# Optimization experiments

Measured on AMD Instinct MI355X. Metric: run time of the kernel, lower is better.

The kernel has to match this reference:

```python
import jax, jax.numpy as jnp
import numpy as np
import math

B, S, E, H = 4, 4096, 2048, 16
Dh = E // H  # 128


def setup_inputs() -> dict:
    key = jax.random.key(0)
    ks = jax.random.split(key, 8)
    s = 1.0 / math.sqrt(E)
    return {
        "x": jax.random.normal(ks[0], (B, S, E), dtype=jnp.float32),
        "Wz": jax.random.uniform(ks[1], (E, E), jnp.float32, -s, s),
        "bz": jax.random.uniform(ks[2], (E,), jnp.float32, -s, s),
        "Wx": jax.random.uniform(ks[3], (E, E), jnp.float32, -s, s),
        "bx": jax.random.uniform(ks[4], (E,), jnp.float32, -s, s),
        "phase": jax.random.normal(ks[5], (H, Dh), dtype=jnp.float32),
        "Wo": jax.random.uniform(ks[6], (E, E), jnp.float32, -s, s),
        "bo": jax.random.uniform(ks[7], (E,), jnp.float32, -s, s),
    }


def reference(x, Wz, bz, Wx, bx, phase, Wo, bo):
    # torch nn.Linear: y = x @ W.T + b  (W stored [out, in])
    z = x @ Wz.T + bz                     # [B,S,E]
    xs = x @ Wx.T + bx                    # [B,S,E]
    z_h = z.reshape(B, S, H, Dh)
    x_h = xs.reshape(B, S, H, Dh)
    # elementwise phase modulation of query heads
    mod = z_h * jnp.sin(phase)            # [B,S,H,Dh] * [H,Dh]
    # NOTE: heads are on axis -2 (no transpose to [B,H,S,Dh]),
    # so scores contract over Dh giving per-token HEAD-mixing: [B,S,H,H]
    scores = jnp.einsum('bshd,bsgd->bshg', mod, x_h) / math.sqrt(Dh)
    w = jax.nn.softmax(scores, axis=-1)   # softmax over head axis g
    att = jnp.einsum('bshg,bsgd->bshd', w, x_h)  # [B,S,H,Dh]
    att = att.reshape(B, S, E)
    return att @ Wo.T + bo
```

## Files before the change

### kernel.cpp

```cpp
#include <hip/hip_runtime.h>
#include <hip/hip_bf16.h>

#define TOK 16384
#define E 2048
#define DH 128

using bf16x8 = __attribute__((ext_vector_type(8))) __bf16;
using f32x4  = __attribute__((ext_vector_type(4))) float;
using u16x8  = __attribute__((ext_vector_type(8))) unsigned short;

static __device__ __forceinline__ unsigned short f2bf(float f) {
  union { float f; unsigned u; } x; x.f = f;
  unsigned r = x.u + 0x7fffu + ((x.u >> 16) & 1u);
  return (unsigned short)(r >> 16);
}

static __device__ __forceinline__ void gload_lds16(const unsigned short* g, unsigned short* l) {
  __builtin_amdgcn_global_load_lds(
      (const __attribute__((address_space(1))) void*)g,
      (__attribute__((address_space(3))) void*)l, 16, 0, 0);
}

__global__ __launch_bounds__(256) void cvt_plain(const float* __restrict__ in,
                                                 unsigned short* __restrict__ out, int n8) {
  int stride = gridDim.x * blockDim.x;
  for (int i = blockIdx.x * blockDim.x + threadIdx.x; i < n8; i += stride) {
    const float4* p = reinterpret_cast<const float4*>(in) + (size_t)i * 2;
    float4 v0 = p[0], v1 = p[1];
    u16x8 o;
    o[0] = f2bf(v0.x); o[1] = f2bf(v0.y); o[2] = f2bf(v0.z); o[3] = f2bf(v0.w);
    o[4] = f2bf(v1.x); o[5] = f2bf(v1.y); o[6] = f2bf(v1.z); o[7] = f2bf(v1.w);
    *(reinterpret_cast<u16x8*>(out) + i) = o;
  }
}

__global__ __launch_bounds__(256) void cvt_scaled(const float* __restrict__ in,
                                                  const float* __restrict__ phase,
                                                  unsigned short* __restrict__ out, int n8) {
  const float rs = 0.08838834764831845f;
  int stride = gridDim.x * blockDim.x;
  for (int i = blockIdx.x * blockDim.x + threadIdx.x; i < n8; i += stride) {
    int row = i >> 8;
    float sc = sinf(phase[row]) * rs;
    const float4* p = reinterpret_cast<const float4*>(in) + (size_t)i * 2;
    float4 v0 = p[0], v1 = p[1];
    u16x8 o;
    o[0] = f2bf(v0.x * sc); o[1] = f2bf(v0.y * sc); o[2] = f2bf(v0.z * sc); o[3] = f2bf(v0.w * sc);
    o[4] = f2bf(v1.x * sc); o[5] = f2bf(v1.y * sc); o[6] = f2bf(v1.z * sc); o[7] = f2bf(v1.w * sc);
    *(reinterpret_cast<u16x8*>(out) + i) = o;
  }
}

__global__ __launch_bounds__(256) void scale_bias(const float* __restrict__ bz,
                                                  const float* __restrict__ phase,
                                                  float* __restrict__ out) {
  const float rs = 0.08838834764831845f;
  int i = blockIdx.x * blockDim.x + threadIdx.x;
  if (i < E) out[i] = bz[i] * sinf(phase[i]) * rs;
}

#define MFMA16 __builtin_amdgcn_mfma_f32_16x16x32_bf16

static __device__ __forceinline__ bf16x8 ldf(const unsigned short* buf, int row, int slot) {
  return *reinterpret_cast<const bf16x8*>(buf + row * 64 + ((slot ^ (row & 7)) << 3));
}

static __device__ __forceinline__ void stage_half(const unsigned short* gbase, int K_,
                                                  unsigned short* dsthalf,
                                                  int r, int slot, int wave) {
#pragma unroll
  for (int c = 0; c < 2; ++c)
    gload_lds16(gbase + (size_t)(c * 64 + r) * K_ + slot * 8,
                dsthalf + c * 4096 + wave * 512);
}

static __device__ __forceinline__ void quad(f32x4 (&acc)[8][4], const bf16x8 (&a)[4][2],
                                            const bf16x8 (&b)[2][2], int mh, int nh) {
#pragma unroll
  for (int mi = 0; mi < 4; ++mi)
#pragma unroll
    for (int ni = 0; ni < 2; ++ni)
#pragma unroll
      for (int kk = 0; kk < 2; ++kk)
        acc[mh * 4 + mi][nh * 2 + ni] =
            MFMA16(a[mi][kk], b[ni][kk], acc[mh * 4 + mi][nh * 2 + ni], 0, 0, 0);
}

#define PH_BAR()  __builtin_amdgcn_s_barrier()
#define PH_LGKM() asm volatile("s_waitcnt lgkmcnt(0)" ::: "memory")
#define PRIO1()   __builtin_amdgcn_s_setprio(1)
#define PRIO0()   __builtin_amdgcn_s_setprio(0)

#define LD_A(dst, buf, base)                                             \
  _Pragma("unroll")                                                      \
  for (int mi = 0; mi < 4; ++mi)                                         \
    _Pragma("unroll")                                                    \
    for (int kk = 0; kk < 2; ++kk)                                       \
      dst[mi][kk] = ldf(buf, (base) + mi * 16, kk * 4 + grp);

#define LD_B(dst, buf, base)                                             \
  _Pragma("unroll")                                                      \
  for (int ni = 0; ni < 2; ++ni)                                         \
    _Pragma("unroll")                                                    \
    for (int kk = 0; kk < 2; ++kk)                                       \
      dst[ni][kk] = ldf(buf, (base) + ni * 16, kk * 4 + grp);

template <bool LAST>
static __device__ __forceinline__ void k_iter(
    const unsigned short* __restrict__ Ag, const unsigned short* __restrict__ Bg,
    int K_, int t,
    unsigned short* sA0, unsigned short* sA1, unsigned short* sB0, unsigned short* sB1,
    int r, int slot, int wave, int grp, int rA, int rB,
    bf16x8 (&bP)[2][2], bf16x8 (&bQ)[2][2], f32x4 (&acc)[8][4]) {
  const size_t k1 = (size_t)(t + 1) * 64, k2 = (size_t)(t + 2) * 64, k3 = (size_t)(t + 3) * 64;
  const size_t hB = (size_t)128 * K_;
  bf16x8 aF[4][2], b1F[2][2];

  LD_A(aF, sA0, rA);
  stage_half(Ag + k1, K_, sA1, r, slot, wave);
  PH_BAR(); PH_LGKM();
  PRIO1(); quad(acc, aF, bP, 0, 0); PRIO0();
  PH_BAR();

  LD_B(b1F, sB0, rB + 32);
  stage_half(Ag + hB + k1, K_, sA1 + 8192, r, slot, wave);
  PH_BAR(); PH_LGKM();
  PRIO1(); quad(acc, aF, b1F, 0, 1); PRIO0();
  PH_BAR();

  LD_A(aF, sA0, rA + 64);
  if (!LAST) stage_half(Bg + k2, K_, sB0, r, slot, wave);
  PH_BAR(); PH_LGKM();
  PRIO1(); quad(acc, aF, b1F, 1, 1); PRIO0();
  PH_BAR();

  if (!LAST) {
    stage_half(Bg + hB + k2, K_, sB0 + 8192, r, slot, wave);
    asm volatile("s_waitcnt vmcnt(4)" ::: "memory");
  } else {
    asm volatile("s_waitcnt vmcnt(0)" ::: "memory");
  }
  PH_BAR();
  PRIO1(); quad(acc, aF, bP, 1, 0); PRIO0();
  LD_B(bQ, sB1, rB);
  PH_BAR();

  LD_A(aF, sA1, rA);
  if (!LAST) stage_half(Ag + k2, K_, sA0, r, slot, wave);
  PH_BAR(); PH_LGKM();
  PRIO1(); quad(acc, aF, bQ, 0, 0); PRIO0();
  PH_BAR();

  LD_B(b1F, sB1, rB + 32);
  if (!LAST) stage_half(Ag + hB + k2, K_, sA0 + 8192, r, slot, wave);
  PH_BAR(); PH_LGKM();
  PRIO1(); quad(acc, aF, b1F, 0, 1); PRIO0();
  PH_BAR();

  LD_A(aF, sA1, rA + 64);
  if (!LAST) stage_half(Bg + k3, K_, sB1, r, slot, wave);
  PH_BAR(); PH_LGKM();
  PRIO1(); quad(acc, aF, b1F, 1, 1); PRIO0();
  PH_BAR();

  if (!LAST) {
    stage_half(Bg + hB + k3, K_, sB1 + 8192, r, slot, wave);
    asm volatile("s_waitcnt vmcnt(4)" ::: "memory");
  }
  PH_BAR();
  PRIO1(); quad(acc, aF, bQ, 1, 0); PRIO0();
  if (!LAST) { LD_B(bP, sB0, rB); }
  PH_BAR();
}

template <bool OUT_BF16>
__global__ __launch_bounds__(512, 2) void gemm256(const unsigned short* __restrict__ A,
                                                  const unsigned short* __restrict__ Bm,
                                                  const float* __restrict__ bias,
                                                  void* __restrict__ C,
                                                  int M, int N, int K_) {
  extern __shared__ unsigned short lds[];
  unsigned short* sA0 = lds;
  unsigned short* sA1 = lds + 16384;
  unsigned short* sB0 = lds + 32768;
  unsigned short* sB1 = lds + 49152;

  const int nbn = N >> 8;
  const int bid = blockIdx.x;
  const int swz = (bid & 7) * ((int)gridDim.x >> 3) + (bid >> 3);
  const int by = swz / nbn, bx = swz % nbn;
  const int tm = by << 8, tn = bx << 8;

  const int tid = threadIdx.x;
  const int wave = tid >> 6, lane = tid & 63;
  const int g16 = lane & 15, grp = lane >> 4;
  const int wm = wave >> 2, wn = wave & 3;
  const int rA = wm * 128 + g16;
  const int rB = wn * 64 + g16;
  const int r = tid >> 3;
  const int slot = (tid & 7) ^ ((tid >> 3) & 7);

  const unsigned short* Ag = A + (size_t)tm * K_;
  const unsigned short* Bg = Bm + (size_t)tn * K_;
  const size_t hB = (size_t)128 * K_;

  f32x4 acc[8][4];
#pragma unroll
  for (int i = 0; i < 8; ++i)
#pragma unroll
    for (int j = 0; j < 4; ++j) acc[i][j] = (f32x4){0.f, 0.f, 0.f, 0.f};

  bf16x8 bP[2][2], bQ[2][2];

  stage_half(Ag, K_, sA0, r, slot, wave);
  stage_half(Ag + hB, K_, sA0 + 8192, r, slot, wave);
  stage_half(Bg, K_, sB0, r, slot, wave);
  stage_half(Bg + hB, K_, sB0 + 8192, r, slot, wave);
  stage_half(Bg + 64, K_, sB1, r, slot, wave);
  stage_half(Bg + hB + 64, K_, sB1 + 8192, r, slot, wave);
  asm volatile("s_waitcnt vmcnt(4)" ::: "memory");
  __builtin_amdgcn_s_barrier();
  LD_B(bP, sB0, rB);

  const int NI = E >> 7;
#pragma unroll 1
  for (int i = 0; i < NI - 1; ++i)
    k_iter<false>(Ag, Bg, K_, 2 * i, sA0, sA1, sB0, sB1, r, slot, wave, grp, rA, rB, bP, bQ, acc);
  k_iter<true>(Ag, Bg, K_, 2 * (NI - 1), sA0, sA1, sB0, sB1, r, slot, wave, grp, rA, rB, bP, bQ, acc);

#pragma unroll
  for (int mi = 0; mi < 8; ++mi) {
#pragma unroll
    for (int ni = 0; ni < 4; ++ni) {
      const int row = tm + wm * 128 + mi * 16 + grp * 4;
      const int col = tn + wn * 64 + ni * 16 + g16;
      const float bv = bias[col];
#pragma unroll
      for (int j = 0; j < 4; ++j) {
        const float v = acc[mi][ni][j] + bv;
        if (OUT_BF16)
          ((unsigned short*)C)[(size_t)(row + j) * N + col] = f2bf(v);
        else
          ((float*)C)[(size_t)(row + j) * N + col] = v;
      }
    }
  }
}

__global__ __launch_bounds__(256) void attn_kernel(const unsigned short* mod,
                                                   const unsigned short* xsg,
                                                   unsigned short* att) {
  __shared__ __align__(16) unsigned short xs_lds[4][16][136];
  __shared__ float w_lds[4][16][17];

  const int wave = threadIdx.x >> 6, lane = threadIdx.x & 63;
  const int token = (blockIdx.x << 2) | wave;
  const unsigned short* modp = mod + (size_t)token * E;
  const unsigned short* xsp  = xsg + (size_t)token * E;
  const int g16 = lane & 15, grp = lane >> 4;

  bf16x8 a[4], b[4];
#pragma unroll
  for (int kk = 0; kk < 4; ++kk) {
    a[kk] = *reinterpret_cast<const bf16x8*>(modp + g16 * DH + kk * 32 + grp * 8);
    b[kk] = *reinterpret_cast<const bf16x8*>(xsp  + g16 * DH + kk * 32 + grp * 8);
  }
#pragma unroll
  for (int kk = 0; kk < 4; ++kk)
    *reinterpret_cast<bf16x8*>(&xs_lds[wave][g16][kk * 32 + grp * 8]) = b[kk];

  f32x4 sc = (f32x4){0.f, 0.f, 0.f, 0.f};
#pragma unroll
  for (int kk = 0; kk < 4; ++kk)
    sc = MFMA16(a[kk], b[kk], sc, 0, 0, 0);

  float w4[4];
#pragma unroll
  for (int j = 0; j < 4; ++j) {
    float s = sc[j];
    float m = s;
#pragma unroll
    for (int off = 1; off < 16; off <<= 1) m = fmaxf(m, __shfl_xor(m, off));
    float e = __expf(s - m);
    float t = e;
#pragma unroll
    for (int off = 1; off < 16; off <<= 1) t += __shfl_xor(t, off);
    w4[j] = e / t;
  }
#pragma unroll
  for (int j = 0; j < 4; ++j) w_lds[wave][grp * 4 + j][g16] = w4[j];

  __syncthreads();

  float acc[32];
#pragma unroll
  for (int i = 0; i < 32; ++i) acc[i] = 0.f;
#pragma unroll
  for (int g = 0; g < 16; ++g) {
    const float wg = w_lds[wave][g16][g];
#pragma unroll
    for (int c = 0; c < 4; ++c) {
      bf16x8 xv = *reinterpret_cast<const bf16x8*>(&xs_lds[wave][g][grp * 32 + c * 8]);
#pragma unroll
      for (int j = 0; j < 8; ++j) acc[c * 8 + j] += wg * (float)xv[j];
    }
  }

  unsigned short* op = att + (size_t)token * E + g16 * DH + grp * 32;
#pragma unroll
  for (int c = 0; c < 4; ++c) {
    u16x8 o;
#pragma unroll
    for (int j = 0; j < 8; ++j) o[j] = f2bf(acc[c * 8 + j]);
    *reinterpret_cast<u16x8*>(op + c * 8) = o;
  }
}

extern "C" void kernel_launch(void* const* d_in, const int* in_sizes, int n_in,
                              void* d_out, int out_size, void* d_ws, size_t ws_size,
                              hipStream_t stream) {
  const float* x     = (const float*)d_in[0];
  const float* Wz    = (const float*)d_in[1];
  const float* bz    = (const float*)d_in[2];
  const float* Wx    = (const float*)d_in[3];
  const float* bx    = (const float*)d_in[4];
  const float* phase = (const float*)d_in[5];
  const float* Wo    = (const float*)d_in[6];
  const float* bo    = (const float*)d_in[7];

  char* p = (char*)d_ws;
  unsigned short* x_bf   = (unsigned short*)p; p += (size_t)TOK * E * 2;
  unsigned short* mod_bf = (unsigned short*)p; p += (size_t)TOK * E * 2;
  unsigned short* xs_bf  = (unsigned short*)p; p += (size_t)TOK * E * 2;
  unsigned short* wz_bf  = (unsigned short*)p; p += (size_t)E * E * 2;
  unsigned short* wx_bf  = (unsigned short*)p; p += (size_t)E * E * 2;
  unsigned short* wo_bf  = (unsigned short*)p; p += (size_t)E * E * 2;
  float* bz_s            = (float*)p;          p += (size_t)E * 4;
  unsigned short* att_bf = mod_bf;

  hipFuncSetAttribute((const void*)gemm256<true>,
                      hipFuncAttributeMaxDynamicSharedMemorySize, 131072);
  hipFuncSetAttribute((const void*)gemm256<false>,
                      hipFuncAttributeMaxDynamicSharedMemorySize, 131072);

  cvt_plain<<<2048, 256, 0, stream>>>(x, x_bf, TOK * E / 8);
  cvt_plain<<<1024, 256, 0, stream>>>(Wx, wx_bf, E * E / 8);
  cvt_plain<<<1024, 256, 0, stream>>>(Wo, wo_bf, E * E / 8);
  cvt_scaled<<<1024, 256, 0, stream>>>(Wz, phase, wz_bf, E * E / 8);
  scale_bias<<<E / 256, 256, 0, stream>>>(bz, phase, bz_s);

  const dim3 ggrid((TOK / 256) * (E / 256));
  gemm256<true><<<ggrid, 512, 131072, stream>>>(x_bf, wz_bf, bz_s, mod_bf, TOK, E, E);
  gemm256<true><<<ggrid, 512, 131072, stream>>>(x_bf, wx_bf, bx, xs_bf, TOK, E, E);
  attn_kernel<<<TOK / 4, 256, 0, stream>>>(mod_bf, xs_bf, att_bf);
  gemm256<false><<<ggrid, 512, 131072, stream>>>(att_bf, wo_bf, bo, (float*)d_out, TOK, E, E);
}
```

Measured before the change: 455.8 us.

## Halve barriers per GEMM k-iteration with finer vmcnt waits

Restructures the 8-phase k-loop schedule so each phase has one barrier instead of two. Each barrier now sits between the LDS fragment reads and the next global-to-LDS stage, with finer vmcnt(4)/vmcnt(2) waits so buffers are confirmed landed just before they are read. The B-fragment prefetch for the next iteration moves earlier. The aim is to cut barrier stalls so MFMA work overlaps better, at the cost of tighter reasoning about buffer hazards and wait counts.

```diff
diff --git a/kernel.cpp b/kernel.cpp
--- a/kernel.cpp
+++ b/kernel.cpp
@@ -88,6 +88,7 @@
 
 #define PH_BAR()  __builtin_amdgcn_s_barrier()
 #define PH_LGKM() asm volatile("s_waitcnt lgkmcnt(0)" ::: "memory")
+#define VMCNT(n)  asm volatile("s_waitcnt vmcnt(" #n ")" ::: "memory")
 #define PRIO1()   __builtin_amdgcn_s_setprio(1)
 #define PRIO0()   __builtin_amdgcn_s_setprio(0)
 
@@ -117,60 +118,58 @@
   bf16x8 aF[4][2], b1F[2][2];
 
   LD_A(aF, sA0, rA);
+  PH_BAR();
   stage_half(Ag + k1, K_, sA1, r, slot, wave);
-  PH_BAR(); PH_LGKM();
+  PH_LGKM();
   PRIO1(); quad(acc, aF, bP, 0, 0); PRIO0();
-  PH_BAR();
 
   LD_B(b1F, sB0, rB + 32);
+  PH_BAR();
   stage_half(Ag + hB + k1, K_, sA1 + 8192, r, slot, wave);
-  PH_BAR(); PH_LGKM();
+  PH_LGKM();
   PRIO1(); quad(acc, aF, b1F, 0, 1); PRIO0();
-  PH_BAR();
 
   LD_A(aF, sA0, rA + 64);
+  VMCNT(4);
+  PH_BAR();
   if (!LAST) stage_half(Bg + k2, K_, sB0, r, slot, wave);
-  PH_BAR(); PH_LGKM();
+  PH_LGKM();
   PRIO1(); quad(acc, aF, b1F, 1, 1); PRIO0();
-  PH_BAR();
+
+  LD_B(bQ, sB1, rB);
+  if (!LAST) { VMCNT(2); } else { VMCNT(0); }
+  PH_BAR();
+  if (!LAST) stage_half(Bg + hB + k2, K_, sB0 + 8192, r, slot, wave);
+  PH_LGKM();
+  PRIO1(); quad(acc, aF, bP, 1, 0); PRIO0();
+
+  LD_A(aF, sA1, rA);
+  PH_BAR();
+  if (!LAST) stage_half(Ag + k2, K_, sA0, r, slot, wave);
+  PH_LGKM();
+  PRIO1(); quad(acc, aF, bQ, 0, 0); PRIO0();
+
+  LD_B(b1F, sB1, rB + 32);
+  PH_BAR();
+  if (!LAST) stage_half(Ag + hB + k2, K_, sA0 + 8192, r, slot, wave);
+  PH_LGKM();
+  PRIO1(); quad(acc, aF, b1F, 0, 1); PRIO0();
+
+  LD_A(aF, sA1, rA + 64);
+  if (!LAST) { VMCNT(4); }
+  PH_BAR();
+  if (!LAST) stage_half(Bg + k3, K_, sB1, r, slot, wave);
+  PH_LGKM();
+  PRIO1(); quad(acc, aF, b1F, 1, 1); PRIO0();
 
   if (!LAST) {
-    stage_half(Bg + hB + k2, K_, sB0 + 8192, r, slot, wave);
-    asm volatile("s_waitcnt vmcnt(4)" ::: "memory");
-  } else {
-    asm volatile("s_waitcnt vmcnt(0)" ::: "memory");
-  }
-  PH_BAR();
-  PRIO1(); quad(acc, aF, bP, 1, 0); PRIO0();
-  LD_B(bQ, sB1, rB);
-  PH_BAR();
-
-  LD_A(aF, sA1, rA);
-  if (!LAST) stage_half(Ag + k2, K_, sA0, r, slot, wave);
-  PH_BAR(); PH_LGKM();
-  PRIO1(); quad(acc, aF, bQ, 0, 0); PRIO0();
-  PH_BAR();
-
-  LD_B(b1F, sB1, rB + 32);
-  if (!LAST) stage_half(Ag + hB + k2, K_, sA0 + 8192, r, slot, wave);
-  PH_BAR(); PH_LGKM();
-  PRIO1(); quad(acc, aF, b1F, 0, 1); PRIO0();
-  PH_BAR();
-
-  LD_A(aF, sA1, rA + 64);
-  if (!LAST) stage_half(Bg + k3, K_, sB1, r, slot, wave);
-  PH_BAR(); PH_LGKM();
-  PRIO1(); quad(acc, aF, b1F, 1, 1); PRIO0();
-  PH_BAR();
-
-  if (!LAST) {
-    stage_half(Bg + hB + k3, K_, sB1 + 8192, r, slot, wave);
-    asm volatile("s_waitcnt vmcnt(4)" ::: "memory");
-  }
-  PH_BAR();
+    LD_B(bP, sB0, rB);
+    VMCNT(2);
+  }
+  PH_BAR();
+  if (!LAST) stage_half(Bg + hB + k3, K_, sB1 + 8192, r, slot, wave);
+  PH_LGKM();
   PRIO1(); quad(acc, aF, bQ, 1, 0); PRIO0();
-  if (!LAST) { LD_B(bP, sB0, rB); }
-  PH_BAR();
 }
 
 template <bool OUT_BF16>
@@ -218,7 +217,7 @@
   stage_half(Bg + hB, K_, sB0 + 8192, r, slot, wave);
   stage_half(Bg + 64, K_, sB1, r, slot, wave);
   stage_half(Bg + hB + 64, K_, sB1 + 8192, r, slot, wave);
-  asm volatile("s_waitcnt vmcnt(4)" ::: "memory");
+  VMCNT(4);
   __builtin_amdgcn_s_barrier();
   LD_B(bP, sB0, rB);
 
```

After: 465.3 us. +2.1%, slower.
